# Performance work log

Measured on AMD Instinct MI355X. Metric: run time of the kernel, lower is better.

Reference implementation:

```python
import jax, jax.numpy as jnp
import numpy as np

N_NODES = 2048
D = 1024
B = 16384
E = 65536

def setup_inputs() -> dict:
    key = jax.random.key(0)
    ks = jax.random.split(key, 8)
    feat = jax.random.normal(ks[0], (B, 7, D), dtype=jnp.float32)
    data_x = jax.random.randint(ks[1], (7 * B,), 0, N_NODES, dtype=jnp.int64)
    adj_rows = jnp.sort(jax.random.randint(ks[2], (E,), 0, N_NODES, dtype=jnp.int32))
    adj_cols = jax.random.randint(ks[3], (E,), 0, N_NODES, dtype=jnp.int32)
    adj_vals = jax.random.uniform(ks[4], (E,), dtype=jnp.float32)
    # kaiming-uniform-like init for GCN weights, zero bias (as in reset_parameters)
    def kaiming(k, fan_in, fan_out):
        bound = jnp.sqrt(6.0 / fan_in)
        return jax.random.uniform(k, (fan_in, fan_out), minval=-bound, maxval=bound, dtype=jnp.float32)
    W1 = kaiming(ks[5], D, N_NODES)
    W2 = kaiming(ks[6], N_NODES, N_NODES)
    W3 = kaiming(ks[7], N_NODES, D)
    return {"feat": feat, "data_x": data_x, "adj_rows": adj_rows, "adj_cols": adj_cols,
            "adj_vals": adj_vals, "W1": W1, "b1": jnp.zeros((N_NODES,), jnp.float32),
            "W2": W2, "b2": jnp.zeros((N_NODES,), jnp.float32),
            "W3": W3, "b3": jnp.zeros((D,), jnp.float32)}

def reference(feat, data_x, adj_rows, adj_cols, adj_vals, W1, b1, W2, b2, W3, b3):
    n = b1.shape[0]  # number of nodes N
    e1 = data_x[0::7]  # [B]
    e2 = data_x[1::7]  # [B]
    # scatter-add: adjacency_matrix[e1] += feat[i,0]; adjacency_matrix[e2] += feat[i,1]
    idx = jnp.concatenate([e1, e2])                       # [2B]
    vals = jnp.concatenate([feat[:, 0, :], feat[:, 1, :]])  # [2B, D]
    node_feat = jax.ops.segment_sum(vals, idx, num_segments=n)  # [N, D]

    def spmm(x):  # sparse [N,N] @ dense [N,F]
        return jax.ops.segment_sum(adj_vals[:, None] * x[adj_cols], adj_rows, num_segments=n)

    h = jax.nn.relu(spmm(node_feat @ W1) + b1)  # [N, N]
    h = spmm(h @ W2) + b2                        # [N, N]
    logits = spmm(h @ W3) + b3                   # [N, D]

    # gather then swap: feat[:,0]=logits[e2], feat[:,1]=logits[e1]
    out = jnp.concatenate([logits[e2][:, None, :], logits[e1][:, None, :], feat[:, 2:, :]], axis=1)
    return out
```

## Files before the change

### kernel.cpp

```cpp
#include <hip/hip_runtime.h>
#include <stdint.h>

#define N_NODES 2048
#define DIM 1024
#define BATCH 16384
#define NEDGE 65536
#define CAP 96

typedef __bf16 bf16x8 __attribute__((ext_vector_type(8)));
typedef float f32x4 __attribute__((ext_vector_type(4)));
typedef unsigned short u16;
typedef unsigned int u32;

__device__ __forceinline__ float bf2f(u16 u) {
  union { u32 i; float f; } v; v.i = ((u32)u) << 16; return v.f;
}
__device__ __forceinline__ u16 f2bf(float f) {
  union { float f; u32 i; } v; v.f = f;
  u32 r = v.i + 0x7fffu + ((v.i >> 16) & 1u);
  return (u16)(r >> 16);
}

__global__ __launch_bounds__(256) void k_bucket(const int* __restrict__ dx,
                                                int* __restrict__ flag,
                                                int* __restrict__ counts,
                                                int* __restrict__ bucket) {
  int is64 = 1;
  for (int j = 0; j < 32; ++j)
    if (dx[2 * j + 1] != 0) { is64 = 0; break; }
  if (blockIdx.x == 0 && threadIdx.x == 0) *flag = is64;
  int i = blockIdx.x * 256 + threadIdx.x;
  if (i >= 2 * BATCH) return;
  long p = (i < BATCH) ? 7L * i : 7L * (i - BATCH) + 1;
  int n = dx[is64 ? 2 * p : p] & (N_NODES - 1);
  int slot = atomicAdd(&counts[n], 1);
  if (slot < CAP) bucket[n * CAP + slot] = i;
}

__global__ __launch_bounds__(256) void k_prep2(const float* __restrict__ feat,
                                               const int* __restrict__ counts,
                                               const int* __restrict__ bucket,
                                               u16* __restrict__ A1,
                                               const int* __restrict__ adj_rows,
                                               int* __restrict__ row_ptr,
                                               const float* __restrict__ W1,
                                               const float* __restrict__ W2,
                                               const float* __restrict__ W3,
                                               u16* __restrict__ Wt1,
                                               u16* __restrict__ Wt2,
                                               u16* __restrict__ Wt3) {
  __shared__ __align__(16) u16 t[32][33];
  int bid = blockIdx.x;
  int tid = threadIdx.x;
  if (bid < 2048) {
    int n = bid;
    int cnt = counts[n]; if (cnt > CAP) cnt = CAP;
    float a0 = 0.f, a1 = 0.f, a2 = 0.f, a3 = 0.f;
    for (int j = 0; j < cnt; ++j) {
      int i = bucket[n * CAP + j];
      size_t rowoff = (i < BATCH) ? ((size_t)i * 7) * DIM
                                  : ((size_t)(i - BATCH) * 7 + 1) * DIM;
      f32x4 v = *(const f32x4*)(feat + rowoff + tid * 4);
      a0 += v[0]; a1 += v[1]; a2 += v[2]; a3 += v[3];
    }
    ushort4 o; o.x = f2bf(a0); o.y = f2bf(a1); o.z = f2bf(a2); o.w = f2bf(a3);
    *(ushort4*)(A1 + (size_t)n * DIM + tid * 4) = o;
    return;
  }
  if (bid < 2057) {
    int r = (bid - 2048) * 256 + tid;
    if (r > N_NODES) return;
    int lo = 0, hi = NEDGE;
    while (lo < hi) { int mid = (lo + hi) >> 1; if (adj_rows[mid] < r) lo = mid + 1; else hi = mid; }
    row_ptr[r] = lo;
    return;
  }
  int tb = bid - 2057;
  const float* W; u16* Wt; int K, N;
  if (tb < 2048)      { W = W1; Wt = Wt1; K = DIM;     N = N_NODES; }
  else if (tb < 6144) { W = W2; Wt = Wt2; K = N_NODES; N = N_NODES; tb -= 2048; }
  else                { W = W3; Wt = Wt3; K = N_NODES; N = DIM;     tb -= 6144; }
  int ntx = N >> 5;
  int bx = tb % ntx;
  int by = tb / ntx;
  int tx = tid & 31, ty = tid >> 5;
  #pragma unroll
  for (int r = 0; r < 32; r += 8)
    t[r + ty][tx] = f2bf(W[(size_t)(by * 32 + r + ty) * N + bx * 32 + tx]);
  __syncthreads();
  #pragma unroll
  for (int r = 0; r < 32; r += 8)
    Wt[(size_t)(bx * 32 + r + ty) * K + by * 32 + tx] = t[tx][r + ty];
}

template <bool F32OUT>
__global__ __launch_bounds__(256) void k_spmm(const u16* __restrict__ X16,
                                              const int* __restrict__ row_ptr,
                                              const int* __restrict__ adj_cols,
                                              const float* __restrict__ adj_vals,
                                              const float* __restrict__ bias,
                                              u16* __restrict__ Y16,
                                              float* __restrict__ Y32,
                                              int width) {
  int chunks = width >> 10;
  int ch = blockIdx.x % chunks;
  int r = blockIdx.x / chunks;
  int col = ch * 1024 + threadIdx.x * 4;
  int e0 = row_ptr[r], e1 = row_ptr[r + 1];
  float a0 = 0.f, a1 = 0.f, a2 = 0.f, a3 = 0.f;
  int e = e0;
  for (; e + 2 <= e1; e += 2) {
    int c0 = adj_cols[e] & (N_NODES - 1);
    int c1 = adj_cols[e + 1] & (N_NODES - 1);
    float v0 = adj_vals[e], v1 = adj_vals[e + 1];
    ushort4 x0 = *(const ushort4*)(X16 + (size_t)c0 * width + col);
    ushort4 x1 = *(const ushort4*)(X16 + (size_t)c1 * width + col);
    a0 += v0 * bf2f(x0.x) + v1 * bf2f(x1.x);
    a1 += v0 * bf2f(x0.y) + v1 * bf2f(x1.y);
    a2 += v0 * bf2f(x0.z) + v1 * bf2f(x1.z);
    a3 += v0 * bf2f(x0.w) + v1 * bf2f(x1.w);
  }
  if (e < e1) {
    int c = adj_cols[e] & (N_NODES - 1);
    float v = adj_vals[e];
    ushort4 x = *(const ushort4*)(X16 + (size_t)c * width + col);
    a0 += v * bf2f(x.x); a1 += v * bf2f(x.y);
    a2 += v * bf2f(x.z); a3 += v * bf2f(x.w);
  }
  if (F32OUT) {
    f32x4 bb = *(const f32x4*)(bias + col);
    f32x4 o; o[0] = a0 + bb[0]; o[1] = a1 + bb[1]; o[2] = a2 + bb[2]; o[3] = a3 + bb[3];
    *(f32x4*)(Y32 + (size_t)r * width + col) = o;
  } else {
    ushort4 o; o.x = f2bf(a0); o.y = f2bf(a1); o.z = f2bf(a2); o.w = f2bf(a3);
    *(ushort4*)(Y16 + (size_t)r * width + col) = o;
  }
}

template <int BM, int BN, int THREADS, bool BIAS, bool RELU>
__global__ __launch_bounds__(THREADS) void k_gemm(const u16* __restrict__ A,
                                                  const u16* __restrict__ Bt,
                                                  const float* __restrict__ bias,
                                                  u16* __restrict__ C16,
                                                  int M, int N, int K) {
  constexpr int BK = 64;
  constexpr int WAVES_N = THREADS / 128;
  constexpr int WM = BM / 2, WN = BN / WAVES_N;
  constexpr int MI = WM / 16, NI = WN / 16;
  constexpr int RPI = THREADS / 8;
  constexpr int IA = BM / RPI, IB = BN / RPI;
  __shared__ __align__(16) u16 As[2][BM * BK];
  __shared__ __align__(16) u16 Bs[2][BN * BK];
  const int ntx = N / BN;
  const int bx = blockIdx.x % ntx;
  const int by = blockIdx.x / ntx;
  const int tid = threadIdx.x;
  const int wid = tid >> 6;
  const int lane = tid & 63;
  const int wr = wid / WAVES_N, wc = wid % WAVES_N;
  const int rowbase = by * BM, colbase = bx * BN;

  f32x4 acc[MI][NI];
  #pragma unroll
  for (int i = 0; i < MI; ++i)
    #pragma unroll
    for (int j = 0; j < NI; ++j) acc[i][j] = (f32x4){0.f, 0.f, 0.f, 0.f};

  const int srow = tid >> 3;
  const int skk = (((tid & 7) ^ (srow & 7)) << 3);

  #define STAGE(buf, kt)                                                        \
    do {                                                                        \
      _Pragma("unroll")                                                         \
      for (int i = 0; i < IA; ++i) {                                            \
        const u16* g = A + (size_t)(rowbase + i * RPI + srow) * K + (kt) + skk; \
        __builtin_amdgcn_global_load_lds(                                       \
            (const __attribute__((address_space(1))) u32*)g,                    \
            (__attribute__((address_space(3))) u32*)(&As[buf][i * (RPI * 64) + tid * 8]), \
            16, 0, 0);                                                          \
      }                                                                         \
      _Pragma("unroll")                                                         \
      for (int i = 0; i < IB; ++i) {                                            \
        const u16* g = Bt + (size_t)(colbase + i * RPI + srow) * K + (kt) + skk;\
        __builtin_amdgcn_global_load_lds(                                       \
            (const __attribute__((address_space(1))) u32*)g,                    \
            (__attribute__((address_space(3))) u32*)(&Bs[buf][i * (RPI * 64) + tid * 8]), \
            16, 0, 0);                                                          \
      }                                                                         \
    } while (0)

  const int rrow = lane & 15;
  const int kq = (lane >> 4) * 8;
  const int rswz = (lane & 7) << 3;

  const int nk = K >> 6;
  STAGE(0, 0);
  __syncthreads();

  for (int t = 0; t < nk; ++t) {
    const u16* as = As[t & 1];
    const u16* bs = Bs[t & 1];
    if (t + 1 < nk) STAGE((t + 1) & 1, (t + 1) << 6);
    bf16x8 af[MI][2], bfr[NI][2];
    #pragma unroll
    for (int mi = 0; mi < MI; ++mi) {
      int r = wr * WM + mi * 16 + rrow;
      #pragma unroll
      for (int h = 0; h < 2; ++h)
        af[mi][h] = *(const bf16x8*)(as + r * 64 + ((h * 32 + kq) ^ rswz));
    }
    #pragma unroll
    for (int ni = 0; ni < NI; ++ni) {
      int c = wc * WN + ni * 16 + rrow;
      #pragma unroll
      for (int h = 0; h < 2; ++h)
        bfr[ni][h] = *(const bf16x8*)(bs + c * 64 + ((h * 32 + kq) ^ rswz));
    }
    #pragma unroll
    for (int h = 0; h < 2; ++h)
      #pragma unroll
      for (int mi = 0; mi < MI; ++mi)
        #pragma unroll
        for (int ni = 0; ni < NI; ++ni)
          acc[mi][ni] = __builtin_amdgcn_mfma_f32_16x16x32_bf16(af[mi][h], bfr[ni][h], acc[mi][ni], 0, 0, 0);
    __syncthreads();
  }
  #undef STAGE

  #pragma unroll
  for (int mi = 0; mi < MI; ++mi) {
    #pragma unroll
    for (int ni = 0; ni < NI; ++ni) {
      int col = colbase + wc * WN + ni * 16 + rrow;
      float bv = BIAS ? bias[col] : 0.f;
      #pragma unroll
      for (int j = 0; j < 4; ++j) {
        int row = rowbase + wr * WM + mi * 16 + (lane >> 4) * 4 + j;
        float v = acc[mi][ni][j] + bv;
        if (RELU) v = fmaxf(v, 0.f);
        C16[(size_t)row * N + col] = f2bf(v);
      }
    }
  }
}

__global__ __launch_bounds__(256) void k_assemble(const float* __restrict__ feat,
                                                  const float* __restrict__ logits,
                                                  const int* __restrict__ dx,
                                                  const int* __restrict__ flag,
                                                  float* __restrict__ out) {
  int i = blockIdx.x;
  int b = i / 7, slot = i - b * 7;
  const float* src;
  if (slot <= 1) {
    int f = *flag;
    long p = 7L * b + (slot == 0 ? 1 : 0);
    int node = dx[f ? 2 * p : p] & (N_NODES - 1);
    src = logits + (size_t)node * DIM;
  } else {
    src = feat + ((size_t)b * 7 + slot) * DIM;
  }
  f32x4 v = *(const f32x4*)(src + threadIdx.x * 4);
  __builtin_nontemporal_store(v, (f32x4*)(out + ((size_t)b * 7 + slot) * DIM + threadIdx.x * 4));
}

extern "C" void kernel_launch(void* const* d_in, const int* in_sizes, int n_in,
                              void* d_out, int out_size, void* d_ws, size_t ws_size,
                              hipStream_t stream) {
  const float* feat   = (const float*)d_in[0];
  const int* data_x   = (const int*)d_in[1];
  const int* adj_rows = (const int*)d_in[2];
  const int* adj_cols = (const int*)d_in[3];
  const float* adj_vals = (const float*)d_in[4];
  const float* W1 = (const float*)d_in[5];
  const float* b1 = (const float*)d_in[6];
  const float* W2 = (const float*)d_in[7];
  const float* b2 = (const float*)d_in[8];
  const float* W3 = (const float*)d_in[9];
  const float* b3 = (const float*)d_in[10];
  float* out = (float*)d_out;

  char* ws = (char*)d_ws;
  size_t off = 0;
  auto alloc = [&](size_t bytes) {
    char* p = ws + off; off += (bytes + 511) & ~(size_t)511; return p;
  };
  int*  flag    = (int*)alloc(4);
  int*  counts  = (int*)alloc(N_NODES * 4);
  int*  bucket  = (int*)alloc((size_t)N_NODES * CAP * 4);
  int*  row_ptr = (int*)alloc((N_NODES + 1) * 4);
  u16*  A1      = (u16*)alloc((size_t)N_NODES * DIM * 2);
  u16*  S       = (u16*)alloc((size_t)N_NODES * N_NODES * 2);
  u16*  H       = (u16*)alloc((size_t)N_NODES * N_NODES * 2);
  u16*  X3      = (u16*)alloc((size_t)N_NODES * DIM * 2);
  u16*  Wt1     = (u16*)alloc((size_t)DIM * N_NODES * 2);
  u16*  Wt2     = (u16*)alloc((size_t)N_NODES * N_NODES * 2);
  u16*  Wt3     = (u16*)alloc((size_t)N_NODES * DIM * 2);
  float* logits = (float*)alloc((size_t)N_NODES * DIM * 4);

  hipMemsetAsync(counts, 0, N_NODES * 4, stream);
  k_bucket<<<(2 * BATCH + 255) / 256, 256, 0, stream>>>(data_x, flag, counts, bucket);
  k_prep2<<<2057 + 8192, 256, 0, stream>>>(feat, counts, bucket, A1, adj_rows, row_ptr,
                                           W1, W2, W3, Wt1, Wt2, Wt3);

  k_spmm<false><<<2048, 256, 0, stream>>>(A1, row_ptr, adj_cols, adj_vals, nullptr, S,
                                          nullptr, DIM);
  k_gemm<128, 128, 512, true, true><<<256, 512, 0, stream>>>(S, Wt1, b1, H, N_NODES, N_NODES, DIM);
  k_spmm<false><<<4096, 256, 0, stream>>>(H, row_ptr, adj_cols, adj_vals, nullptr, S,
                                          nullptr, N_NODES);
  k_gemm<128, 128, 512, true, false><<<256, 512, 0, stream>>>(S, Wt2, b2, H, N_NODES, N_NODES, N_NODES);
  k_gemm<128, 64, 256, false, false><<<256, 256, 0, stream>>>(H, Wt3, nullptr, X3, N_NODES, DIM, N_NODES);
  k_spmm<true><<<2048, 256, 0, stream>>>(X3, row_ptr, adj_cols, adj_vals, b3, nullptr,
                                         logits, DIM);

  k_assemble<<<BATCH * 7, 256, 0, stream>>>(feat, logits, data_x, flag, out);
}
```

Baseline: 317.6 us.

## Fuse SpMM/GEMM chain into persistent kernel with grid barriers and overlapped feat copy

Replaces the six separate SpMM and GEMM launches with one persistent kernel of 256 compute blocks that run each stage as tile loops separated by atomic grid barriers. A further 256 blocks in the same launch copy the pass-through feat slots 2..6 into the output at the same time. The final assemble kernel now only gathers the two logits slots. The aim is to cut launch gaps and overlap the large memory-bound copy with the compute chain. In exchange, the GEMMs now use 256-thread blocks on 128x128 tiles, where they used to use 512-thread blocks, and the barriers assume all 256 compute blocks are resident at once.

```diff
diff --git a/kernel.cpp b/kernel.cpp
--- a/kernel.cpp
+++ b/kernel.cpp
@@ -6,6 +6,8 @@
 #define BATCH 16384
 #define NEDGE 65536
 #define CAP 96
+#define NC 256
+#define NCOPY 256
 
 typedef __bf16 bf16x8 __attribute__((ext_vector_type(8)));
 typedef float f32x4 __attribute__((ext_vector_type(4)));
@@ -19,6 +21,18 @@
   union { float f; u32 i; } v; v.f = f;
   u32 r = v.i + 0x7fffu + ((v.i >> 16) & 1u);
   return (u16)(r >> 16);
+}
+
+__device__ __forceinline__ void copy_feat_rows(const float* __restrict__ feat,
+                                               float* __restrict__ out,
+                                               int row0, int tid) {
+  #pragma unroll 4
+  for (int t = row0; t < row0 + 32; ++t) {
+    int b = t / 5, s = t - b * 5 + 2;
+    size_t o = ((size_t)b * 7 + s) * DIM + tid * 4;
+    f32x4 v = __builtin_nontemporal_load((const f32x4*)(feat + o));
+    __builtin_nontemporal_store(v, (f32x4*)(out + o));
+  }
 }
 
 __global__ __launch_bounds__(256) void k_bucket(const int* __restrict__ dx,
@@ -94,17 +108,17 @@
 }
 
 template <bool F32OUT>
-__global__ __launch_bounds__(256) void k_spmm(const u16* __restrict__ X16,
-                                              const int* __restrict__ row_ptr,
-                                              const int* __restrict__ adj_cols,
-                                              const float* __restrict__ adj_vals,
-                                              const float* __restrict__ bias,
-                                              u16* __restrict__ Y16,
-                                              float* __restrict__ Y32,
-                                              int width) {
+__device__ __forceinline__ void spmm_task(const u16* __restrict__ X16,
+                                          const int* __restrict__ row_ptr,
+                                          const int* __restrict__ adj_cols,
+                                          const float* __restrict__ adj_vals,
+                                          const float* __restrict__ bias,
+                                          u16* __restrict__ Y16,
+                                          float* __restrict__ Y32,
+                                          int width, int task) {
   int chunks = width >> 10;
-  int ch = blockIdx.x % chunks;
-  int r = blockIdx.x / chunks;
+  int ch = task % chunks;
+  int r = task / chunks;
   int col = ch * 1024 + threadIdx.x * 4;
   int e0 = row_ptr[r], e1 = row_ptr[r + 1];
   float a0 = 0.f, a1 = 0.f, a2 = 0.f, a3 = 0.f;
@@ -137,54 +151,47 @@
   }
 }
 
-template <int BM, int BN, int THREADS, bool BIAS, bool RELU>
-__global__ __launch_bounds__(THREADS) void k_gemm(const u16* __restrict__ A,
-                                                  const u16* __restrict__ Bt,
-                                                  const float* __restrict__ bias,
-                                                  u16* __restrict__ C16,
-                                                  int M, int N, int K) {
-  constexpr int BK = 64;
-  constexpr int WAVES_N = THREADS / 128;
-  constexpr int WM = BM / 2, WN = BN / WAVES_N;
-  constexpr int MI = WM / 16, NI = WN / 16;
-  constexpr int RPI = THREADS / 8;
-  constexpr int IA = BM / RPI, IB = BN / RPI;
-  __shared__ __align__(16) u16 As[2][BM * BK];
-  __shared__ __align__(16) u16 Bs[2][BN * BK];
-  const int ntx = N / BN;
-  const int bx = blockIdx.x % ntx;
-  const int by = blockIdx.x / ntx;
+template <bool BIAS, bool RELU>
+__device__ __forceinline__ void gemm_tile(const u16* __restrict__ A,
+                                          const u16* __restrict__ Bt,
+                                          const float* __restrict__ bias,
+                                          u16* __restrict__ C16,
+                                          int N, int K, int tile,
+                                          u16* As0, u16* Bs0) {
+  const int ntx = N >> 7;
+  const int bx = tile % ntx;
+  const int by = tile / ntx;
   const int tid = threadIdx.x;
   const int wid = tid >> 6;
   const int lane = tid & 63;
-  const int wr = wid / WAVES_N, wc = wid % WAVES_N;
-  const int rowbase = by * BM, colbase = bx * BN;
-
-  f32x4 acc[MI][NI];
+  const int wr = wid >> 1, wc = wid & 1;
+  const int rowbase = by * 128, colbase = bx * 128;
+
+  f32x4 acc[4][4];
   #pragma unroll
-  for (int i = 0; i < MI; ++i)
-    #pragma unroll
-    for (int j = 0; j < NI; ++j) acc[i][j] = (f32x4){0.f, 0.f, 0.f, 0.f};
+  for (int i = 0; i < 4; ++i)
+    #pragma unroll
+    for (int j = 0; j < 4; ++j) acc[i][j] = (f32x4){0.f, 0.f, 0.f, 0.f};
 
   const int srow = tid >> 3;
   const int skk = (((tid & 7) ^ (srow & 7)) << 3);
 
-  #define STAGE(buf, kt)                                                        \
+  #define MSTAGE(buf, kt)                                                       \
     do {                                                                        \
       _Pragma("unroll")                                                         \
-      for (int i = 0; i < IA; ++i) {                                            \
-        const u16* g = A + (size_t)(rowbase + i * RPI + srow) * K + (kt) + skk; \
+      for (int i = 0; i < 4; ++i) {                                             \
+        const u16* g = A + (size_t)(rowbase + i * 32 + srow) * K + (kt) + skk;  \
         __builtin_amdgcn_global_load_lds(                                       \
             (const __attribute__((address_space(1))) u32*)g,                    \
-            (__attribute__((address_space(3))) u32*)(&As[buf][i * (RPI * 64) + tid * 8]), \
+            (__attribute__((address_space(3))) u32*)(As0 + (buf) * 8192 + i * 2048 + tid * 8), \
             16, 0, 0);                                                          \
       }                                                                         \
       _Pragma("unroll")                                                         \
-      for (int i = 0; i < IB; ++i) {                                            \
-        const u16* g = Bt + (size_t)(colbase + i * RPI + srow) * K + (kt) + skk;\
+      for (int i = 0; i < 4; ++i) {                                             \
+        const u16* g = Bt + (size_t)(colbase + i * 32 + srow) * K + (kt) + skk; \
         __builtin_amdgcn_global_load_lds(                                       \
             (const __attribute__((address_space(1))) u32*)g,                    \
-            (__attribute__((address_space(3))) u32*)(&Bs[buf][i * (RPI * 64) + tid * 8]), \
+            (__attribute__((address_space(3))) u32*)(Bs0 + (buf) * 8192 + i * 2048 + tid * 8), \
             16, 0, 0);                                                          \
       }                                                                         \
     } while (0)
@@ -194,24 +201,24 @@
   const int rswz = (lane & 7) << 3;
 
   const int nk = K >> 6;
-  STAGE(0, 0);
+  MSTAGE(0, 0);
   __syncthreads();
 
   for (int t = 0; t < nk; ++t) {
-    const u16* as = As[t & 1];
-    const u16* bs = Bs[t & 1];
-    if (t + 1 < nk) STAGE((t + 1) & 1, (t + 1) << 6);
-    bf16x8 af[MI][2], bfr[NI][2];
-    #pragma unroll
-    for (int mi = 0; mi < MI; ++mi) {
-      int r = wr * WM + mi * 16 + rrow;
+    const u16* as = As0 + (t & 1) * 8192;
+    const u16* bs = Bs0 + (t & 1) * 8192;
+    if (t + 1 < nk) MSTAGE((t + 1) & 1, (t + 1) << 6);
+    bf16x8 af[4][2], bfr[4][2];
+    #pragma unroll
+    for (int mi = 0; mi < 4; ++mi) {
+      int r = wr * 64 + mi * 16 + rrow;
       #pragma unroll
       for (int h = 0; h < 2; ++h)
         af[mi][h] = *(const bf16x8*)(as + r * 64 + ((h * 32 + kq) ^ rswz));
     }
     #pragma unroll
-    for (int ni = 0; ni < NI; ++ni) {
-      int c = wc * WN + ni * 16 + rrow;
+    for (int ni = 0; ni < 4; ++ni) {
+      int c = wc * 64 + ni * 16 + rrow;
       #pragma unroll
       for (int h = 0; h < 2; ++h)
         bfr[ni][h] = *(const bf16x8*)(bs + c * 64 + ((h * 32 + kq) ^ rswz));
@@ -219,23 +226,23 @@
     #pragma unroll
     for (int h = 0; h < 2; ++h)
       #pragma unroll
-      for (int mi = 0; mi < MI; ++mi)
+      for (int mi = 0; mi < 4; ++mi)
         #pragma unroll
-        for (int ni = 0; ni < NI; ++ni)
+        for (int ni = 0; ni < 4; ++ni)
           acc[mi][ni] = __builtin_amdgcn_mfma_f32_16x16x32_bf16(af[mi][h], bfr[ni][h], acc[mi][ni], 0, 0, 0);
     __syncthreads();
   }
-  #undef STAGE
+  #undef MSTAGE
 
   #pragma unroll
-  for (int mi = 0; mi < MI; ++mi) {
-    #pragma unroll
-    for (int ni = 0; ni < NI; ++ni) {
-      int col = colbase + wc * WN + ni * 16 + rrow;
+  for (int mi = 0; mi < 4; ++mi) {
+    #pragma unroll
+    for (int ni = 0; ni < 4; ++ni) {
+      int col = colbase + wc * 64 + ni * 16 + rrow;
       float bv = BIAS ? bias[col] : 0.f;
       #pragma unroll
       for (int j = 0; j < 4; ++j) {
-        int row = rowbase + wr * WM + mi * 16 + (lane >> 4) * 4 + j;
+        int row = rowbase + wr * 64 + mi * 16 + (lane >> 4) * 4 + j;
         float v = acc[mi][ni][j] + bv;
         if (RELU) v = fmaxf(v, 0.f);
         C16[(size_t)row * N + col] = f2bf(v);
@@ -244,23 +251,64 @@
   }
 }
 
-__global__ __launch_bounds__(256) void k_assemble(const float* __restrict__ feat,
-                                                  const float* __restrict__ logits,
-                                                  const int* __restrict__ dx,
-                                                  const int* __restrict__ flag,
-                                                  float* __restrict__ out) {
+__device__ __forceinline__ void xbar(int* sync, int p) {
+  __syncthreads();
+  if (threadIdx.x == 0) {
+    __builtin_amdgcn_fence(__ATOMIC_RELEASE, "agent");
+    __hip_atomic_fetch_add(&sync[p], 1, __ATOMIC_RELAXED, __HIP_MEMORY_SCOPE_AGENT);
+    while (__hip_atomic_load(&sync[p], __ATOMIC_RELAXED, __HIP_MEMORY_SCOPE_AGENT) < NC)
+      __builtin_amdgcn_s_sleep(8);
+    __builtin_amdgcn_fence(__ATOMIC_ACQUIRE, "agent");
+  }
+  __syncthreads();
+}
+
+__global__ __launch_bounds__(256, 2) void k_mega(
+    const u16* __restrict__ A1, u16* __restrict__ S, u16* __restrict__ H,
+    u16* __restrict__ X3, float* __restrict__ logits,
+    const u16* __restrict__ Wt1, const u16* __restrict__ Wt2, const u16* __restrict__ Wt3,
+    const float* __restrict__ b1, const float* __restrict__ b2, const float* __restrict__ b3,
+    const int* __restrict__ row_ptr, const int* __restrict__ adj_cols,
+    const float* __restrict__ adj_vals,
+    const float* __restrict__ feat, float* __restrict__ out,
+    int* __restrict__ sync) {
+  __shared__ __align__(16) u16 AsB[2 * 8192];
+  __shared__ __align__(16) u16 BsB[2 * 8192];
+  const int bid = blockIdx.x;
+  if (bid >= NC) {
+    for (int t = bid - NC; t < 2560; t += NCOPY)
+      copy_feat_rows(feat, out, t * 32, threadIdx.x);
+    return;
+  }
+  for (int t = bid; t < 2048; t += NC)
+    spmm_task<false>(A1, row_ptr, adj_cols, adj_vals, nullptr, S, nullptr, DIM, t);
+  xbar(sync, 0);
+  for (int t = bid; t < 256; t += NC)
+    gemm_tile<true, true>(S, Wt1, b1, H, N_NODES, DIM, t, AsB, BsB);
+  xbar(sync, 1);
+  for (int t = bid; t < 4096; t += NC)
+    spmm_task<false>(H, row_ptr, adj_cols, adj_vals, nullptr, S, nullptr, N_NODES, t);
+  xbar(sync, 2);
+  for (int t = bid; t < 256; t += NC)
+    gemm_tile<true, false>(S, Wt2, b2, H, N_NODES, N_NODES, t, AsB, BsB);
+  xbar(sync, 3);
+  for (int t = bid; t < 128; t += NC)
+    gemm_tile<false, false>(H, Wt3, nullptr, X3, DIM, N_NODES, t, AsB, BsB);
+  xbar(sync, 4);
+  for (int t = bid; t < 2048; t += NC)
+    spmm_task<true>(X3, row_ptr, adj_cols, adj_vals, b3, nullptr, logits, DIM, t);
+}
+
+__global__ __launch_bounds__(256) void k_assemble2(const float* __restrict__ logits,
+                                                   const int* __restrict__ dx,
+                                                   const int* __restrict__ flag,
+                                                   float* __restrict__ out) {
   int i = blockIdx.x;
-  int b = i / 7, slot = i - b * 7;
-  const float* src;
-  if (slot <= 1) {
-    int f = *flag;
-    long p = 7L * b + (slot == 0 ? 1 : 0);
-    int node = dx[f ? 2 * p : p] & (N_NODES - 1);
-    src = logits + (size_t)node * DIM;
-  } else {
-    src = feat + ((size_t)b * 7 + slot) * DIM;
-  }
-  f32x4 v = *(const f32x4*)(src + threadIdx.x * 4);
+  int b = i >> 1, slot = i & 1;
+  int f = *flag;
+  long p = 7L * b + (slot == 0 ? 1 : 0);
+  int node = dx[f ? 2 * p : p] & (N_NODES - 1);
+  f32x4 v = *(const f32x4*)(logits + (size_t)node * DIM + threadIdx.x * 4);
   __builtin_nontemporal_store(v, (f32x4*)(out + ((size_t)b * 7 + slot) * DIM + threadIdx.x * 4));
 }
 
@@ -286,6 +334,7 @@
     char* p = ws + off; off += (bytes + 511) & ~(size_t)511; return p;
   };
   int*  flag    = (int*)alloc(4);
+  int*  sync    = (int*)alloc(32);
   int*  counts  = (int*)alloc(N_NODES * 4);
   int*  bucket  = (int*)alloc((size_t)N_NODES * CAP * 4);
   int*  row_ptr = (int*)alloc((N_NODES + 1) * 4);
@@ -299,19 +348,12 @@
   float* logits = (float*)alloc((size_t)N_NODES * DIM * 4);
 
   hipMemsetAsync(counts, 0, N_NODES * 4, stream);
+  hipMemsetAsync(sync, 0, 32, stream);
   k_bucket<<<(2 * BATCH + 255) / 256, 256, 0, stream>>>(data_x, flag, counts, bucket);
   k_prep2<<<2057 + 8192, 256, 0, stream>>>(feat, counts, bucket, A1, adj_rows, row_ptr,
                                            W1, W2, W3, Wt1, Wt2, Wt3);
-
-  k_spmm<false><<<2048, 256, 0, stream>>>(A1, row_ptr, adj_cols, adj_vals, nullptr, S,
-                                          nullptr, DIM);
-  k_gemm<128, 128, 512, true, true><<<256, 512, 0, stream>>>(S, Wt1, b1, H, N_NODES, N_NODES, DIM);
-  k_spmm<false><<<4096, 256, 0, stream>>>(H, row_ptr, adj_cols, adj_vals, nullptr, S,
-                                          nullptr, N_NODES);
-  k_gemm<128, 128, 512, true, false><<<256, 512, 0, stream>>>(S, Wt2, b2, H, N_NODES, N_NODES, N_NODES);
-  k_gemm<128, 64, 256, false, false><<<256, 256, 0, stream>>>(H, Wt3, nullptr, X3, N_NODES, DIM, N_NODES);
-  k_spmm<true><<<2048, 256, 0, stream>>>(X3, row_ptr, adj_cols, adj_vals, b3, nullptr,
-                                         logits, DIM);
-
-  k_assemble<<<BATCH * 7, 256, 0, stream>>>(feat, logits, data_x, flag, out);
-}
+  k_mega<<<NC + NCOPY, 256, 0, stream>>>(A1, S, H, X3, logits, Wt1, Wt2, Wt3,
+                                         b1, b2, b3, row_ptr, adj_cols, adj_vals,
+                                         feat, out, sync);
+  k_assemble2<<<2 * BATCH, 256, 0, stream>>>(logits, data_x, flag, out);
+}
```

Result: slower. 520.1 us (+63.7%).
